# Performance work log

Measured on AMD Instinct MI355X. Metric: run time of the kernel, lower is better.

## Reference

```python
import jax, jax.numpy as jnp
import numpy as np

H = 2048          # hidden_size
NQ = 16           # num_q_heads
NKV = 4           # num_kv_heads
HD = H // NQ      # head_dim = 128
REP = NQ // NKV   # kv repeat factor
FF = 8192         # intermediate_size
B, S = 2, 2048
EPS = 1e-6


def setup_inputs() -> dict:
    key = jax.random.key(0)
    ks = jax.random.split(key, 12)
    sd = 0.02
    return {
        "hidden_states": jax.random.normal(ks[0], (B, S, H), jnp.float32),
        "Wq": jax.random.normal(ks[1], (H, H), jnp.float32) * sd,
        "bq": jnp.zeros((H,), jnp.float32),
        "Wk": jax.random.normal(ks[2], (H, NKV * HD), jnp.float32) * sd,
        "bk": jnp.zeros((NKV * HD,), jnp.float32),
        "Wv": jax.random.normal(ks[3], (H, NKV * HD), jnp.float32) * sd,
        "bv": jnp.zeros((NKV * HD,), jnp.float32),
        "Wo": jax.random.normal(ks[4], (H, H), jnp.float32) * sd,
        "bo": jnp.zeros((H,), jnp.float32),
        "W1": jax.random.normal(ks[5], (H, FF), jnp.float32) * sd,
        "b1": jnp.zeros((FF,), jnp.float32),
        "W2": jax.random.normal(ks[6], (FF, H), jnp.float32) * sd,
        "b2": jnp.zeros((H,), jnp.float32),
        "g1": jnp.ones((H,), jnp.float32),  # ln1 weight
        "g2": jnp.ones((H,), jnp.float32),  # ln2 weight
    }


def _rmsnorm(x, g):
    rms = jnp.sqrt(jnp.mean(x * x, axis=-1, keepdims=True) + EPS)
    return g * (x / rms)


def _attention(x, Wq, bq, Wk, bk, Wv, bv, Wo, bo):
    b, s, _ = x.shape
    q = (x @ Wq + bq).reshape(b, s, NQ, HD).transpose(0, 2, 1, 3)    # [b,hq,s,d]
    k = (x @ Wk + bk).reshape(b, s, NKV, HD).transpose(0, 2, 1, 3)   # [b,hkv,s,d]
    v = (x @ Wv + bv).reshape(b, s, NKV, HD).transpose(0, 2, 1, 3)
    k = jnp.repeat(k, REP, axis=1)  # GQA: repeat_interleave over head dim
    v = jnp.repeat(v, REP, axis=1)
    scale = 1.0 / np.sqrt(HD).astype(np.float32)
    scores = jnp.einsum("bhqd,bhkd->bhqk", q, k) * scale
    causal = jnp.triu(jnp.ones((s, s), bool), k=1)                   # True above diag
    scores = jnp.where(causal[None, None], -jnp.inf, scores)
    probs = jax.nn.softmax(scores, axis=-1)
    ctx = jnp.einsum("bhqk,bhkd->bhqd", probs, v)
    ctx = ctx.transpose(0, 2, 1, 3).reshape(b, s, H)
    return ctx @ Wo + bo


def reference(hidden_states, Wq, bq, Wk, bk, Wv, bv, Wo, bo, W1, b1, W2, b2, g1, g2):
    x = hidden_states
    # pre-norm attention block
    x = x + _attention(_rmsnorm(x, g1), Wq, bq, Wk, bk, Wv, bv, Wo, bo)
    # pre-norm FFN block (exact GELU, matching torch nn.GELU default)
    h = _rmsnorm(x, g2)
    h = jax.nn.gelu(h @ W1 + b1, approximate=False) @ W2 + b2
    return x + h
```

## Files before the change

### kernel.cpp

```cpp
#include <hip/hip_runtime.h>
#include <cstdint>

#define H_    2048
#define NQ_   16
#define NKV_  4
#define HD_   128
#define FF_   8192
#define B_    2
#define S_    2048
#define TOK   (B_*S_)
#define QKVN  (H_ + 2*NKV_*HD_)

typedef __bf16 bf16;
typedef bf16  bf16x8 __attribute__((ext_vector_type(8)));
typedef float f32x4  __attribute__((ext_vector_type(4)));

typedef __attribute__((address_space(1))) void as1_void;
typedef __attribute__((address_space(3))) void as3_void;

__device__ __forceinline__ void gload_lds16(const void* g, void* l) {
    __builtin_amdgcn_global_load_lds((as1_void*)g, (as3_void*)l, 16, 0, 0);
}

__global__ __launch_bounds__(256) void wtrans_kernel(
    const float* __restrict__ W, bf16* __restrict__ Wt, int K, int N, int outOff)
{
    __shared__ float tile[32][33];
    const int n0 = (int)blockIdx.x * 32;
    const int k0 = (int)blockIdx.y * 32;
    const int c  = (int)threadIdx.x & 31;
    const int r  = (int)threadIdx.x >> 5;
#pragma unroll
    for (int i = 0; i < 4; ++i)
        tile[r + i*8][c] = W[(size_t)(k0 + r + i*8) * N + n0 + c];
    __syncthreads();
#pragma unroll
    for (int i = 0; i < 4; ++i)
        Wt[(size_t)(outOff + n0 + r + i*8) * K + k0 + c] = (bf16)tile[c][r + i*8];
}

__global__ void biaspack_kernel(const float* __restrict__ bq, const float* __restrict__ bk,
                                const float* __restrict__ bv, float* __restrict__ out)
{
    const int i = (int)(blockIdx.x * 256 + threadIdx.x);
    out[i] = (i < H_) ? bq[i] : (i < H_ + NKV_*HD_ ? bk[i - H_] : bv[i - H_ - NKV_*HD_]);
}

__global__ __launch_bounds__(256) void rmsnorm_kernel(
    const float* __restrict__ x, const float* __restrict__ g, bf16* __restrict__ y)
{
    const int row = (int)blockIdx.x;
    const int tid = (int)threadIdx.x;
    const float* xr = x + (size_t)row * H_;
    const float4 a = *(const float4*)(xr + tid*8);
    const float4 c = *(const float4*)(xr + tid*8 + 4);
    float ss = a.x*a.x + a.y*a.y + a.z*a.z + a.w*a.w
             + c.x*c.x + c.y*c.y + c.z*c.z + c.w*c.w;
#pragma unroll
    for (int d = 1; d < 64; d <<= 1) ss += __shfl_xor(ss, d);
    __shared__ float red[4];
    if ((tid & 63) == 0) red[tid >> 6] = ss;
    __syncthreads();
    const float inv = rsqrtf((red[0]+red[1]+red[2]+red[3]) * (1.0f/H_) + 1e-6f);
    const float vals[8] = {a.x,a.y,a.z,a.w,c.x,c.y,c.z,c.w};
    const float* gp = g + tid*8;
    bf16x8 outv;
#pragma unroll
    for (int e = 0; e < 8; ++e) outv[e] = (bf16)(vals[e] * inv * gp[e]);
    *(bf16x8*)(y + (size_t)row * H_ + tid*8) = outv;
}

template<int MODE>
__global__ __launch_bounds__(256) void gemm_kernel(
    const bf16* __restrict__ A, const bf16* __restrict__ Bt,
    const float* __restrict__ bias, const float* __restrict__ resid,
    void* __restrict__ Cout, int M, int N, int K)
{
    __shared__ bf16 lA[128*64];
    __shared__ bf16 lB[128*64];
    const int tid  = (int)threadIdx.x;
    const int wid  = tid >> 6;
    const int lane = tid & 63;
    const int lr   = lane & 15;
    const int lg   = lane >> 4;
    const int m0 = (int)blockIdx.y * 128;
    const int n0 = (int)blockIdx.x * 128;
    const int wm = (wid >> 1) * 64;
    const int wn = (wid & 1) * 64;

    f32x4 acc[4][4] = {};

    const int sRow = wid*32 + (lane >> 3);
    const int sCol = ((lane & 7) ^ (lane >> 3)) * 8;
    const bf16* aSrc = A  + (size_t)(m0 + sRow) * K + sCol;
    const bf16* bSrc = Bt + (size_t)(n0 + sRow) * K + sCol;

    for (int k0 = 0; k0 < K; k0 += 64) {
#pragma unroll
        for (int i = 0; i < 4; ++i) {
            gload_lds16(aSrc + (size_t)(i*8)*K + k0, &lA[(wid*32 + i*8)*64]);
            gload_lds16(bSrc + (size_t)(i*8)*K + k0, &lB[(wid*32 + i*8)*64]);
        }
        __syncthreads();
#pragma unroll
        for (int kk = 0; kk < 64; kk += 32) {
            const int ks = (kk + lg*8) ^ ((lr & 7) * 8);
            bf16x8 af[4], bfr[4];
#pragma unroll
            for (int i = 0; i < 4; ++i)
                af[i] = *(const bf16x8*)&lA[(wm + i*16 + lr)*64 + ks];
#pragma unroll
            for (int j = 0; j < 4; ++j)
                bfr[j] = *(const bf16x8*)&lB[(wn + j*16 + lr)*64 + ks];
#pragma unroll
            for (int i = 0; i < 4; ++i)
#pragma unroll
                for (int j = 0; j < 4; ++j)
                    acc[i][j] = __builtin_amdgcn_mfma_f32_16x16x32_bf16(
                        af[i], bfr[j], acc[i][j], 0, 0, 0);
        }
        __syncthreads();
    }

#pragma unroll
    for (int j = 0; j < 4; ++j) {
        const int col = n0 + wn + j*16 + lr;
        const float bj = bias[col];
#pragma unroll
        for (int i = 0; i < 4; ++i) {
            const int row0 = m0 + wm + i*16 + lg*4;
#pragma unroll
            for (int rr = 0; rr < 4; ++rr) {
                float v = acc[i][j][rr] + bj;
                const size_t idx = (size_t)(row0 + rr) * N + col;
                if (MODE == 2) {
                    ((float*)Cout)[idx] = v + resid[idx];
                } else {
                    if (MODE == 1) v = 0.5f * v * (1.0f + erff(v * 0.70710678118654752f));
                    ((bf16*)Cout)[idx] = (bf16)v;
                }
            }
        }
    }
}

__global__ __launch_bounds__(256) void attn_kernel(
    const bf16* __restrict__ qkv, bf16* __restrict__ ctx)
{
    __shared__ bf16 lK[32*128];
    __shared__ bf16 lV[128*40];
    __shared__ bf16 lP[4][16*40];
    const int tid  = (int)threadIdx.x;
    const int wid  = tid >> 6;
    const int lane = tid & 63;
    const int lr   = lane & 15;
    const int lg   = lane >> 4;
    const int qt = (int)blockIdx.x, h = (int)blockIdx.y, b = (int)blockIdx.z;
    const int kh = h >> 2;
    const int qb = qt * 64;
    const int qw = qb + wid * 16;
    const float scale = 0.08838834764831845f;

    bf16x8 qf[4];
    {
        const bf16* qp = qkv + (size_t)(b*S_ + qw + lr) * QKVN + h*HD_ + lg*8;
#pragma unroll
        for (int t = 0; t < 4; ++t) qf[t] = *(const bf16x8*)(qp + t*32);
    }
    f32x4 o[8] = {};
    float mrow[4] = {-__builtin_inff(), -__builtin_inff(), -__builtin_inff(), -__builtin_inff()};
    float lrow[4] = {0.f, 0.f, 0.f, 0.f};

    for (int kv0 = 0; kv0 < qb + 64; kv0 += 32) {
        __syncthreads();
#pragma unroll
        for (int i = 0; i < 2; ++i) {
            const int c   = wid*2 + i;
            const int row = c*4 + lg;
            const int ce  = (lr ^ (row & 7)) * 8;
            gload_lds16(qkv + (size_t)(b*S_ + kv0 + row) * QKVN + H_ + kh*HD_ + ce,
                        &lK[c*4*128]);
        }
        {
            const int r  = tid >> 3;
            const int e0 = (tid & 7) * 16;
            const bf16* vp = qkv + (size_t)(b*S_ + kv0 + r) * QKVN + H_ + NKV_*HD_ + kh*HD_ + e0;
            const bf16x8 v0 = *(const bf16x8*)vp;
            const bf16x8 v1 = *(const bf16x8*)(vp + 8);
#pragma unroll
            for (int e = 0; e < 8; ++e) {
                lV[(e0 + e)*40 + r]     = v0[e];
                lV[(e0 + 8 + e)*40 + r] = v1[e];
            }
        }
        __syncthreads();

        f32x4 s[2] = {};
#pragma unroll
        for (int sub = 0; sub < 2; ++sub) {
            const int krow = sub*16 + lr;
#pragma unroll
            for (int t = 0; t < 4; ++t) {
                const int ks = (t*32 + lg*8) ^ ((krow & 7) * 8);
                const bf16x8 kf = *(const bf16x8*)&lK[krow*128 + ks];
                s[sub] = __builtin_amdgcn_mfma_f32_16x16x32_bf16(qf[t], kf, s[sub], 0, 0, 0);
            }
        }
        float p[2][4], rmax[4];
#pragma unroll
        for (int rr = 0; rr < 4; ++rr) {
            const int q = qw + lg*4 + rr;
#pragma unroll
            for (int sub = 0; sub < 2; ++sub) {
                const int kv = kv0 + sub*16 + lr;
                const float v = s[sub][rr] * scale;
                p[sub][rr] = (kv <= q) ? v : -__builtin_inff();
            }
            rmax[rr] = fmaxf(p[0][rr], p[1][rr]);
        }
#pragma unroll
        for (int d = 1; d < 16; d <<= 1)
#pragma unroll
            for (int rr = 0; rr < 4; ++rr)
                rmax[rr] = fmaxf(rmax[rr], __shfl_xor(rmax[rr], d));
        float fsc[4], rsum[4];
#pragma unroll
        for (int rr = 0; rr < 4; ++rr) {
            const float mn = fmaxf(mrow[rr], rmax[rr]);
            fsc[rr]  = __expf(mrow[rr] - mn);
            mrow[rr] = mn;
            p[0][rr] = __expf(p[0][rr] - mn);
            p[1][rr] = __expf(p[1][rr] - mn);
            rsum[rr] = p[0][rr] + p[1][rr];
        }
#pragma unroll
        for (int d = 1; d < 16; d <<= 1)
#pragma unroll
            for (int rr = 0; rr < 4; ++rr)
                rsum[rr] += __shfl_xor(rsum[rr], d);
#pragma unroll
        for (int rr = 0; rr < 4; ++rr) lrow[rr] = lrow[rr]*fsc[rr] + rsum[rr];
#pragma unroll
        for (int t = 0; t < 8; ++t)
#pragma unroll
            for (int rr = 0; rr < 4; ++rr) o[t][rr] *= fsc[rr];
#pragma unroll
        for (int sub = 0; sub < 2; ++sub)
#pragma unroll
            for (int rr = 0; rr < 4; ++rr)
                lP[wid][(lg*4 + rr)*40 + sub*16 + lr] = (bf16)p[sub][rr];
        const bf16x8 pf = *(const bf16x8*)&lP[wid][lr*40 + lg*8];
#pragma unroll
        for (int t = 0; t < 8; ++t) {
            const bf16x8 vf = *(const bf16x8*)&lV[(t*16 + lr)*40 + lg*8];
            o[t] = __builtin_amdgcn_mfma_f32_16x16x32_bf16(pf, vf, o[t], 0, 0, 0);
        }
    }
#pragma unroll
    for (int rr = 0; rr < 4; ++rr) {
        const float inv = 1.0f / lrow[rr];
        bf16* cp = ctx + (size_t)(b*S_ + qw + lg*4 + rr) * H_ + h*HD_ + lr;
#pragma unroll
        for (int t = 0; t < 8; ++t)
            cp[t*16] = (bf16)(o[t][rr] * inv);
    }
}

extern "C" void kernel_launch(void* const* d_in, const int* in_sizes, int n_in,
                              void* d_out, int out_size, void* d_ws, size_t ws_size,
                              hipStream_t stream)
{
    const float* hidden = (const float*)d_in[0];
    const float* Wq = (const float*)d_in[1];
    const float* bq = (const float*)d_in[2];
    const float* Wk = (const float*)d_in[3];
    const float* bk = (const float*)d_in[4];
    const float* Wv = (const float*)d_in[5];
    const float* bv = (const float*)d_in[6];
    const float* Wo = (const float*)d_in[7];
    const float* bo = (const float*)d_in[8];
    const float* W1 = (const float*)d_in[9];
    const float* b1 = (const float*)d_in[10];
    const float* W2 = (const float*)d_in[11];
    const float* b2 = (const float*)d_in[12];
    const float* g1 = (const float*)d_in[13];
    const float* g2 = (const float*)d_in[14];
    float* out = (float*)d_out;

    char* p = (char*)d_ws;
    auto alloc = [&](size_t bytes) { char* r = p; p += (bytes + 255) & ~(size_t)255; return r; };
    bf16*  wt_qkv = (bf16*)alloc((size_t)QKVN * H_ * 2);
    bf16*  wo_t   = (bf16*)alloc((size_t)H_ * H_ * 2);
    bf16*  w1_t   = (bf16*)alloc((size_t)FF_ * H_ * 2);
    bf16*  w2_t   = (bf16*)alloc((size_t)H_ * FF_ * 2);
    float* bqkv   = (float*)alloc((size_t)QKVN * 4);
    bf16*  xn1    = (bf16*)alloc((size_t)TOK * H_ * 2);
    bf16*  qkv    = (bf16*)alloc((size_t)TOK * QKVN * 2);
    bf16*  ctxb   = (bf16*)alloc((size_t)TOK * H_ * 2);
    float* x1     = (float*)alloc((size_t)TOK * H_ * 4);
    bf16*  xn2    = (bf16*)alloc((size_t)TOK * H_ * 2);
    bf16*  ffn    = (bf16*)alloc((size_t)TOK * FF_ * 2);

    const dim3 blk(256);
    biaspack_kernel<<<dim3(QKVN/256), blk, 0, stream>>>(bq, bk, bv, bqkv);
    wtrans_kernel<<<dim3(H_/32,  H_/32),  blk, 0, stream>>>(Wq, wt_qkv, H_, H_,  0);
    wtrans_kernel<<<dim3(512/32, H_/32),  blk, 0, stream>>>(Wk, wt_qkv, H_, 512, H_);
    wtrans_kernel<<<dim3(512/32, H_/32),  blk, 0, stream>>>(Wv, wt_qkv, H_, 512, H_ + 512);
    wtrans_kernel<<<dim3(H_/32,  H_/32),  blk, 0, stream>>>(Wo, wo_t,   H_, H_,  0);
    wtrans_kernel<<<dim3(FF_/32, H_/32),  blk, 0, stream>>>(W1, w1_t,   H_, FF_, 0);
    wtrans_kernel<<<dim3(H_/32,  FF_/32), blk, 0, stream>>>(W2, w2_t,   FF_, H_, 0);

    rmsnorm_kernel<<<dim3(TOK), blk, 0, stream>>>(hidden, g1, xn1);
    gemm_kernel<0><<<dim3(QKVN/128, TOK/128), blk, 0, stream>>>(
        xn1, wt_qkv, bqkv, nullptr, qkv, TOK, QKVN, H_);
    attn_kernel<<<dim3(S_/64, NQ_, B_), blk, 0, stream>>>(qkv, ctxb);
    gemm_kernel<2><<<dim3(H_/128, TOK/128), blk, 0, stream>>>(
        ctxb, wo_t, bo, hidden, x1, TOK, H_, H_);
    rmsnorm_kernel<<<dim3(TOK), blk, 0, stream>>>(x1, g2, xn2);
    gemm_kernel<1><<<dim3(FF_/128, TOK/128), blk, 0, stream>>>(
        xn2, w1_t, b1, nullptr, ffn, TOK, FF_, H_);
    gemm_kernel<2><<<dim3(H_/128, TOK/128), blk, 0, stream>>>(
        ffn, w2_t, b2, x1, out, TOK, H_, FF_);
}
```

Baseline: 910.7 us.

## Double-buffer attention KV tiles with async LDS loads and pre-transposed V

Adds a separate kernel that transposes V into a per-kv-head [d][s] buffer, reusing the xn1 workspace, so attention can load V tiles with direct global-to-LDS loads instead of a scalar scatter-transpose. The attention kernel now processes 64-wide KV tiles with double-buffered K and V in LDS, prefetching the next tile while computing the current one. The causal mask is applied only on the diagonal tile, and query tiles are launched in reverse order so the longest blocks start first. The cost is an extra launch and a transpose pass over V, plus more LDS per block, which may lower occupancy.

Result: faster. 758.1 us (-16.8%).

```diff
diff --git a/kernel.cpp b/kernel.cpp
--- a/kernel.cpp
+++ b/kernel.cpp
@@ -10,6 +10,7 @@
 #define S_    2048
 #define TOK   (B_*S_)
 #define QKVN  (H_ + 2*NKV_*HD_)
+#define KVB   64
 
 typedef __bf16 bf16;
 typedef bf16  bf16x8 __attribute__((ext_vector_type(8)));
@@ -68,6 +69,26 @@
 #pragma unroll
     for (int e = 0; e < 8; ++e) outv[e] = (bf16)(vals[e] * inv * gp[e]);
     *(bf16x8*)(y + (size_t)row * H_ + tid*8) = outv;
+}
+
+__global__ __launch_bounds__(256) void vtrans_kernel(
+    const bf16* __restrict__ qkv, bf16* __restrict__ Vt)
+{
+    __shared__ bf16 tile[32][33];
+    const int tt = (int)blockIdx.x;
+    const int d0 = (int)blockIdx.y * 32;
+    const int kh = (int)blockIdx.z;
+    const int b  = (tt*32) / S_;
+    const int s0 = (tt*32) % S_;
+    const int c = (int)threadIdx.x & 31;
+    const int r = (int)threadIdx.x >> 5;
+#pragma unroll
+    for (int i = 0; i < 4; ++i)
+        tile[r + i*8][c] = qkv[(size_t)(tt*32 + r + i*8)*QKVN + H_ + NKV_*HD_ + kh*HD_ + d0 + c];
+    __syncthreads();
+#pragma unroll
+    for (int i = 0; i < 4; ++i)
+        Vt[((size_t)(b*NKV_ + kh)*HD_ + d0 + r + i*8)*S_ + s0 + c] = tile[c][r + i*8];
 }
 
 template<int MODE>
@@ -145,93 +166,124 @@
 }
 
 __global__ __launch_bounds__(256) void attn_kernel(
-    const bf16* __restrict__ qkv, bf16* __restrict__ ctx)
-{
-    __shared__ bf16 lK[32*128];
-    __shared__ bf16 lV[128*40];
-    __shared__ bf16 lP[4][16*40];
+    const bf16* __restrict__ qkv, const bf16* __restrict__ Vt,
+    bf16* __restrict__ ctx)
+{
+    __shared__ bf16 lK[2][KVB*HD_];
+    __shared__ bf16 lV[2][HD_*KVB];
+    __shared__ bf16 lP[4][16*72];
     const int tid  = (int)threadIdx.x;
     const int wid  = tid >> 6;
     const int lane = tid & 63;
     const int lr   = lane & 15;
     const int lg   = lane >> 4;
-    const int qt = (int)blockIdx.x, h = (int)blockIdx.y, b = (int)blockIdx.z;
+    const int qt = (int)gridDim.x - 1 - (int)blockIdx.x;
+    const int h = (int)blockIdx.y, b = (int)blockIdx.z;
     const int kh = h >> 2;
     const int qb = qt * 64;
     const int qw = qb + wid * 16;
     const float scale = 0.08838834764831845f;
 
+    const bf16* kB[4];
+    const bf16* vB[4];
+#pragma unroll
+    for (int i = 0; i < 4; ++i) {
+        const int kRow = (wid*4 + i)*4 + (lane >> 4);
+        const int kCol = ((lane & 15) ^ (kRow & 7)) * 8;
+        kB[i] = qkv + (size_t)(b*S_ + kRow)*QKVN + H_ + kh*HD_ + kCol;
+        const int vRow = (wid*4 + i)*8 + (lane >> 3);
+        const int vCol = ((lane & 7) ^ (vRow & 7)) * 8;
+        vB[i] = Vt + ((size_t)(b*NKV_ + kh)*HD_ + vRow)*S_ + vCol;
+    }
+
     bf16x8 qf[4];
     {
-        const bf16* qp = qkv + (size_t)(b*S_ + qw + lr) * QKVN + h*HD_ + lg*8;
+        const bf16* qp = qkv + (size_t)(b*S_ + qw + lr)*QKVN + h*HD_ + lg*8;
 #pragma unroll
         for (int t = 0; t < 4; ++t) qf[t] = *(const bf16x8*)(qp + t*32);
     }
+
     f32x4 o[8] = {};
     float mrow[4] = {-__builtin_inff(), -__builtin_inff(), -__builtin_inff(), -__builtin_inff()};
     float lrow[4] = {0.f, 0.f, 0.f, 0.f};
-
-    for (int kv0 = 0; kv0 < qb + 64; kv0 += 32) {
+    const int nt = qt + 1;
+
+#pragma unroll
+    for (int i = 0; i < 4; ++i) {
+        gload_lds16(kB[i], &lK[0][(wid*4 + i)*4*HD_]);
+        gload_lds16(vB[i], &lV[0][(wid*4 + i)*8*KVB]);
+    }
+
+    int cur = 0;
+    for (int t = 0; t < nt; ++t) {
         __syncthreads();
-#pragma unroll
-        for (int i = 0; i < 2; ++i) {
-            const int c   = wid*2 + i;
-            const int row = c*4 + lg;
-            const int ce  = (lr ^ (row & 7)) * 8;
-            gload_lds16(qkv + (size_t)(b*S_ + kv0 + row) * QKVN + H_ + kh*HD_ + ce,
-                        &lK[c*4*128]);
-        }
-        {
-            const int r  = tid >> 3;
-            const int e0 = (tid & 7) * 16;
-            const bf16* vp = qkv + (size_t)(b*S_ + kv0 + r) * QKVN + H_ + NKV_*HD_ + kh*HD_ + e0;
-            const bf16x8 v0 = *(const bf16x8*)vp;
-            const bf16x8 v1 = *(const bf16x8*)(vp + 8);
-#pragma unroll
-            for (int e = 0; e < 8; ++e) {
-                lV[(e0 + e)*40 + r]     = v0[e];
-                lV[(e0 + 8 + e)*40 + r] = v1[e];
-            }
-        }
-        __syncthreads();
-
-        f32x4 s[2] = {};
-#pragma unroll
-        for (int sub = 0; sub < 2; ++sub) {
+        if (t + 1 < nt) {
+            const size_t kAdd = (size_t)(t+1)*KVB*QKVN;
+            const size_t vAdd = (size_t)(t+1)*KVB;
+#pragma unroll
+            for (int i = 0; i < 4; ++i) {
+                gload_lds16(kB[i] + kAdd, &lK[cur^1][(wid*4 + i)*4*HD_]);
+                gload_lds16(vB[i] + vAdd, &lV[cur^1][(wid*4 + i)*8*KVB]);
+            }
+        }
+        const int kv0 = t * KVB;
+
+        f32x4 s[4] = {};
+#pragma unroll
+        for (int sub = 0; sub < 4; ++sub) {
             const int krow = sub*16 + lr;
-#pragma unroll
-            for (int t = 0; t < 4; ++t) {
-                const int ks = (t*32 + lg*8) ^ ((krow & 7) * 8);
-                const bf16x8 kf = *(const bf16x8*)&lK[krow*128 + ks];
-                s[sub] = __builtin_amdgcn_mfma_f32_16x16x32_bf16(qf[t], kf, s[sub], 0, 0, 0);
-            }
-        }
-        float p[2][4], rmax[4];
-#pragma unroll
-        for (int rr = 0; rr < 4; ++rr) {
-            const int q = qw + lg*4 + rr;
-#pragma unroll
-            for (int sub = 0; sub < 2; ++sub) {
-                const int kv = kv0 + sub*16 + lr;
-                const float v = s[sub][rr] * scale;
-                p[sub][rr] = (kv <= q) ? v : -__builtin_inff();
-            }
-            rmax[rr] = fmaxf(p[0][rr], p[1][rr]);
+            const bf16* kr = &lK[cur][krow*HD_];
+            const int sw = (krow & 7) * 8;
+#pragma unroll
+            for (int d = 0; d < 4; ++d) {
+                const bf16x8 kf = *(const bf16x8*)(kr + ((d*32 + lg*8) ^ sw));
+                s[sub] = __builtin_amdgcn_mfma_f32_16x16x32_bf16(qf[d], kf, s[sub], 0, 0, 0);
+            }
+        }
+
+        float p[4][4], rmax[4];
+        if (t == qt) {
+#pragma unroll
+            for (int rr = 0; rr < 4; ++rr) {
+                const int q = qw + lg*4 + rr;
+                rmax[rr] = -__builtin_inff();
+#pragma unroll
+                for (int sub = 0; sub < 4; ++sub) {
+                    const int kv = kv0 + sub*16 + lr;
+                    const float v = s[sub][rr] * scale;
+                    p[sub][rr] = (kv <= q) ? v : -__builtin_inff();
+                    rmax[rr] = fmaxf(rmax[rr], p[sub][rr]);
+                }
+            }
+        } else {
+#pragma unroll
+            for (int rr = 0; rr < 4; ++rr) {
+                rmax[rr] = -__builtin_inff();
+#pragma unroll
+                for (int sub = 0; sub < 4; ++sub) {
+                    p[sub][rr] = s[sub][rr] * scale;
+                    rmax[rr] = fmaxf(rmax[rr], p[sub][rr]);
+                }
+            }
         }
 #pragma unroll
         for (int d = 1; d < 16; d <<= 1)
 #pragma unroll
             for (int rr = 0; rr < 4; ++rr)
                 rmax[rr] = fmaxf(rmax[rr], __shfl_xor(rmax[rr], d));
+
         float fsc[4], rsum[4];
 #pragma unroll
         for (int rr = 0; rr < 4; ++rr) {
             const float mn = fmaxf(mrow[rr], rmax[rr]);
             fsc[rr]  = __expf(mrow[rr] - mn);
             mrow[rr] = mn;
-            p[0][rr] = __expf(p[0][rr] - mn);
-            p[1][rr] = __expf(p[1][rr] - mn);
-            rsum[rr] = p[0][rr] + p[1][rr];
+            rsum[rr] = 0.f;
+#pragma unroll
+            for (int sub = 0; sub < 4; ++sub) {
+                p[sub][rr] = __expf(p[sub][rr] - mn);
+                rsum[rr] += p[sub][rr];
+            }
         }
 #pragma unroll
         for (int d = 1; d < 16; d <<= 1)
@@ -241,28 +293,40 @@
 #pragma unroll
         for (int rr = 0; rr < 4; ++rr) lrow[rr] = lrow[rr]*fsc[rr] + rsum[rr];
 #pragma unroll
-        for (int t = 0; t < 8; ++t)
-#pragma unroll
-            for (int rr = 0; rr < 4; ++rr) o[t][rr] *= fsc[rr];
-#pragma unroll
-        for (int sub = 0; sub < 2; ++sub)
+        for (int dch = 0; dch < 8; ++dch)
+#pragma unroll
+            for (int rr = 0; rr < 4; ++rr) o[dch][rr] *= fsc[rr];
+
+#pragma unroll
+        for (int sub = 0; sub < 4; ++sub)
 #pragma unroll
             for (int rr = 0; rr < 4; ++rr)
-                lP[wid][(lg*4 + rr)*40 + sub*16 + lr] = (bf16)p[sub][rr];
-        const bf16x8 pf = *(const bf16x8*)&lP[wid][lr*40 + lg*8];
-#pragma unroll
-        for (int t = 0; t < 8; ++t) {
-            const bf16x8 vf = *(const bf16x8*)&lV[(t*16 + lr)*40 + lg*8];
-            o[t] = __builtin_amdgcn_mfma_f32_16x16x32_bf16(pf, vf, o[t], 0, 0, 0);
-        }
-    }
+                lP[wid][(lg*4 + rr)*72 + sub*16 + lr] = (bf16)p[sub][rr];
+        bf16x8 pf[2];
+#pragma unroll
+        for (int kk = 0; kk < 2; ++kk)
+            pf[kk] = *(const bf16x8*)&lP[wid][lr*72 + kk*32 + lg*8];
+
+#pragma unroll
+        for (int dch = 0; dch < 8; ++dch) {
+            const bf16* vr = &lV[cur][(dch*16 + lr)*KVB];
+            const int sw = (lr & 7) * 8;
+#pragma unroll
+            for (int kk = 0; kk < 2; ++kk) {
+                const bf16x8 vf = *(const bf16x8*)(vr + ((kk*32 + lg*8) ^ sw));
+                o[dch] = __builtin_amdgcn_mfma_f32_16x16x32_bf16(pf[kk], vf, o[dch], 0, 0, 0);
+            }
+        }
+        cur ^= 1;
+    }
+
 #pragma unroll
     for (int rr = 0; rr < 4; ++rr) {
         const float inv = 1.0f / lrow[rr];
         bf16* cp = ctx + (size_t)(b*S_ + qw + lg*4 + rr) * H_ + h*HD_ + lr;
 #pragma unroll
-        for (int t = 0; t < 8; ++t)
-            cp[t*16] = (bf16)(o[t][rr] * inv);
+        for (int dch = 0; dch < 8; ++dch)
+            cp[dch*16] = (bf16)(o[dch][rr] * inv);
     }
 }
 
@@ -300,6 +364,7 @@
     float* x1     = (float*)alloc((size_t)TOK * H_ * 4);
     bf16*  xn2    = (bf16*)alloc((size_t)TOK * H_ * 2);
     bf16*  ffn    = (bf16*)alloc((size_t)TOK * FF_ * 2);
+    bf16*  vt     = xn1;
 
     const dim3 blk(256);
     biaspack_kernel<<<dim3(QKVN/256), blk, 0, stream>>>(bq, bk, bv, bqkv);
@@ -313,7 +378,8 @@
     rmsnorm_kernel<<<dim3(TOK), blk, 0, stream>>>(hidden, g1, xn1);
     gemm_kernel<0><<<dim3(QKVN/128, TOK/128), blk, 0, stream>>>(
         xn1, wt_qkv, bqkv, nullptr, qkv, TOK, QKVN, H_);
-    attn_kernel<<<dim3(S_/64, NQ_, B_), blk, 0, stream>>>(qkv, ctxb);
+    vtrans_kernel<<<dim3(TOK/32, HD_/32, NKV_), blk, 0, stream>>>(qkv, vt);
+    attn_kernel<<<dim3(S_/64, NQ_, B_), blk, 0, stream>>>(qkv, vt, ctxb);
     gemm_kernel<2><<<dim3(H_/128, TOK/128), blk, 0, stream>>>(
         ctxb, wo_t, bo, hidden, x1, TOK, H_, H_);
     rmsnorm_kernel<<<dim3(TOK), blk, 0, stream>>>(x1, g2, xn2);
```
